# Kernel optimization log

Measured on AMD Instinct MI355X. Metric: run time of the kernel, lower is better.

Reference implementation:

```python
import jax, jax.numpy as jnp
import numpy as np
from jax import lax

B, T, D, H, O = 256, 256, 128, 1024, 128


def setup_inputs() -> dict:
    key = jax.random.key(0)
    ks = jax.random.split(key, 13)
    s = 1.0 / np.sqrt(H)  # torch LSTMCell/Linear init scale
    return {
        "x": jax.random.normal(ks[0], (B, T, D), jnp.float32),
        "h0": jax.random.normal(ks[1], (B, H), jnp.float32),
        "c0": jax.random.normal(ks[2], (B, H), jnp.float32),
        "W_ih0": jax.random.uniform(ks[3], (4 * H, D), jnp.float32, -s, s),
        "W_hh0": jax.random.uniform(ks[4], (4 * H, H), jnp.float32, -s, s),
        "b_ih0": jax.random.uniform(ks[5], (4 * H,), jnp.float32, -s, s),
        "b_hh0": jax.random.uniform(ks[6], (4 * H,), jnp.float32, -s, s),
        "W_ih1": jax.random.uniform(ks[7], (4 * H, H), jnp.float32, -s, s),
        "W_hh1": jax.random.uniform(ks[8], (4 * H, H), jnp.float32, -s, s),
        "b_ih1": jax.random.uniform(ks[9], (4 * H,), jnp.float32, -s, s),
        "b_hh1": jax.random.uniform(ks[10], (4 * H,), jnp.float32, -s, s),
        "W_out": jax.random.uniform(ks[11], (O, H), jnp.float32, -s, s),
        "b_out": jax.random.uniform(ks[12], (O,), jnp.float32, -s, s),
    }


def _lstm_cell(xin, h, c, W_ih, W_hh, b_ih, b_hh):
    # gates in torch order: input, forget, cell(g), output
    g = xin @ W_ih.T + b_ih + h @ W_hh.T + b_hh  # [B, 4H]
    i, f, gg, o = jnp.split(g, 4, axis=-1)
    c_new = jax.nn.sigmoid(f) * c + jax.nn.sigmoid(i) * jnp.tanh(gg)
    h_new = jax.nn.sigmoid(o) * jnp.tanh(c_new)
    return h_new, c_new


def reference(x, h0, c0, W_ih0, W_hh0, b_ih0, b_hh0,
              W_ih1, W_hh1, b_ih1, b_hh1, W_out, b_out):
    xt = jnp.transpose(x, (1, 0, 2))  # [T, B, D] time-major

    def step(carry, xin):
        (ha, ca), (hb, cb) = carry
        ha, ca = _lstm_cell(xin, ha, ca, W_ih0, W_hh0, b_ih0, b_hh0)
        hb, cb = _lstm_cell(ha, hb, cb, W_ih1, W_hh1, b_ih1, b_hh1)
        return ((ha, ca), (hb, cb)), None

    # same initial (h, c) tuple replicated to both layers, as in the original
    init = ((h0, c0), (h0, c0))
    carry, _ = lax.scan(step, init, xt)
    h_last = carry[1][0]  # top-layer hidden at final step, [B, H]
    return h_last @ W_out.T + b_out  # [B, O]
```

## Files before the change

### kernel.cpp

```cpp
#include <hip/hip_runtime.h>
#include <hip/hip_fp16.h>


#define Bq 256
#define Hq 1024

typedef _Float16 half8 __attribute__((ext_vector_type(8)));
typedef float    floatx4 __attribute__((ext_vector_type(4)));

#define N_W1 8388608LL
#define N_W0 4718592LL
#define N_XH 8388608LL
#define N_H  262144LL
#define BH   262144

#define OFF_W1 0LL
#define OFF_W0 16777216LL
#define OFF_XH 26214400LL
#define OFF_BA 42991616LL
#define OFF_BB 44040192LL
#define OFF_HF 45088768LL
#define OFF_SY 46137344LL
#define REQ_WS 46139392LL

__global__ void ws_sentinel_kernel(float* __restrict__ out, int n, float v)
{
    int i = blockIdx.x * blockDim.x + threadIdx.x;
    if (i < n) out[i] = v;
}

__global__ void prep_kernel(const float* __restrict__ x, const float* __restrict__ h0,
                            const float* __restrict__ Wih0, const float* __restrict__ Whh0,
                            const float* __restrict__ Wih1, const float* __restrict__ Whh1,
                            _Float16* __restrict__ w1p, _Float16* __restrict__ w0p,
                            _Float16* __restrict__ xh,
                            _Float16* __restrict__ bufA, _Float16* __restrict__ bufB,
                            unsigned* __restrict__ sync)
{
    long long gid = (long long)blockIdx.x * blockDim.x + threadIdx.x;
    if (gid < 512) sync[gid] = 0u;

    if (gid < N_W1) {
        long long i = gid;
        int e  = (int)(i & 7);
        int jj = (int)((i >> 3) & 15);
        int n  = (int)((i >> 7) & 1);
        int kb = (int)((i >> 8) & 3);
        int ks = (int)((i >> 10) & 63);
        int cb = (int)(i >> 16);
        int row = (2 * n + (jj >> 3)) * 1024 + cb * 8 + (jj & 7);
        int k = ks * 32 + kb * 8 + e;
        float v = (k < 1024) ? Wih1[(size_t)row * 1024 + k]
                             : Whh1[(size_t)row * 1024 + (k - 1024)];
        w1p[i] = (_Float16)v;
    } else if (gid < N_W1 + N_W0) {
        long long i = gid - N_W1;
        int cb = (int)(i / 36864LL);
        int r  = (int)(i - (long long)cb * 36864LL);
        int ks = r >> 10;
        int kb = (r >> 8) & 3;
        int n  = (r >> 7) & 1;
        int jj = (r >> 3) & 15;
        int e  = r & 7;
        int row = (2 * n + (jj >> 3)) * 1024 + cb * 8 + (jj & 7);
        int k = ks * 32 + kb * 8 + e;
        float v = (k < 128) ? Wih0[(size_t)row * 128 + k]
                            : Whh0[(size_t)row * 1024 + (k - 128)];
        w0p[i] = (_Float16)v;
    } else if (gid < N_W1 + N_W0 + N_XH) {
        long long i = gid - N_W1 - N_W0;
        int t    = (int)(i >> 15);
        int rem  = (int)(i & 32767);
        int tile = rem >> 13;
        int b    = (rem >> 5) & 255;
        int e    = rem & 31;
        int d    = tile * 32 + e;
        xh[i] = (_Float16)x[((size_t)b * 256 + t) * 128 + d];
    } else if (gid < N_W1 + N_W0 + N_XH + N_H) {
        long long i = gid - N_W1 - N_W0 - N_XH;
        int row = (int)(i >> 10);
        int j   = (int)(i & 1023);
        size_t idx = (size_t)(j >> 5) * 8192 + (size_t)row * 32 + (j & 31);
        _Float16 v = (_Float16)h0[i];
        bufA[BH + idx] = v;
        bufB[BH + idx] = v;
    }
}

__device__ __forceinline__ void phasebar(unsigned* flags, unsigned* xcdgo,
                                         int bid, int slot, unsigned target)
{
    __builtin_amdgcn_s_waitcnt(0);
    __syncthreads();
    if (threadIdx.x == 0)
        __hip_atomic_store(flags + bid, target, __ATOMIC_RELAXED,
                           __HIP_MEMORY_SCOPE_AGENT);
    if (slot == 0) {
        if (threadIdx.x < 256) {
            int guard = 0;
            while (__hip_atomic_load(flags + threadIdx.x, __ATOMIC_RELAXED,
                                     __HIP_MEMORY_SCOPE_AGENT) < target) {
                __builtin_amdgcn_s_sleep(1);
                if (++guard > (1 << 18)) break;
            }
        }
        __syncthreads();
        if (threadIdx.x < 64) {
            __builtin_amdgcn_fence(__ATOMIC_ACQUIRE, "agent");
            asm volatile("s_waitcnt vmcnt(0) lgkmcnt(0)" ::: "memory");
            if (threadIdx.x == 0)
                __hip_atomic_store(xcdgo, target, __ATOMIC_RELAXED,
                                   __HIP_MEMORY_SCOPE_AGENT);
        }
        __syncthreads();
    } else {
        if (threadIdx.x == 0) {
            int guard = 0;
            while (__hip_atomic_load(xcdgo, __ATOMIC_RELAXED,
                                     __HIP_MEMORY_SCOPE_AGENT) < target) {
                __builtin_amdgcn_s_sleep(1);
                if (++guard > (1 << 18)) break;
            }
        }
        __syncthreads();
        if (threadIdx.x == 0) {
            asm volatile("buffer_inv" ::: "memory");
            asm volatile("s_waitcnt vmcnt(0)" ::: "memory");
        }
        __syncthreads();
    }
}

#define MFMA16(A, Bv, C) __builtin_amdgcn_mfma_f32_16x16x32_f16((A), (Bv), (C), 0, 0, 0)

#define PISSUE(I, P0, P1)                                           \
    asm volatile("global_load_dwordx4 %0, %2, off\n\t"              \
                 "global_load_dwordx4 %1, %3, off"                  \
                 : "=&v"(bf[I][0]), "=&v"(bf[I][1])                 \
                 : "v"(P0), "v"(P1) : "memory")

#define PSTEP22(I, P0, P1) do {                                     \
    half8 b0 = *(const half8*)(bp);                                 \
    half8 b1 = *(const half8*)(bp + 128);                           \
    asm volatile("s_waitcnt vmcnt(22)" ::: "memory");               \
    __builtin_amdgcn_sched_barrier(0);                              \
    acc[0][0] = MFMA16(bf[I][0], b0, acc[0][0]);                    \
    acc[0][1] = MFMA16(bf[I][0], b1, acc[0][1]);                    \
    acc[1][0] = MFMA16(bf[I][1], b0, acc[1][0]);                    \
    acc[1][1] = MFMA16(bf[I][1], b1, acc[1][1]);                    \
    bp += 1024;                                                     \
    PISSUE(I, P0, P1);                                              \
} while (0)

#define PSTEPW(I, NLIT) do {                                        \
    half8 b0 = *(const half8*)(bp);                                 \
    half8 b1 = *(const half8*)(bp + 128);                           \
    asm volatile("s_waitcnt vmcnt(" #NLIT ")" ::: "memory");        \
    __builtin_amdgcn_sched_barrier(0);                              \
    acc[0][0] = MFMA16(bf[I][0], b0, acc[0][0]);                    \
    acc[0][1] = MFMA16(bf[I][0], b1, acc[0][1]);                    \
    acc[1][0] = MFMA16(bf[I][1], b0, acc[1][0]);                    \
    acc[1][1] = MFMA16(bf[I][1], b1, acc[1][1]);                    \
    bp += 1024;                                                     \
} while (0)

__global__ void __launch_bounds__(512)
lstm_main(const _Float16* __restrict__ w1p, const _Float16* __restrict__ w0p,
          const _Float16* __restrict__ xh,
          _Float16* __restrict__ bufA, _Float16* __restrict__ bufB,
          float* __restrict__ hbF,
          const float* __restrict__ c0,
          const float* __restrict__ bih0, const float* __restrict__ bhh0,
          const float* __restrict__ bih1, const float* __restrict__ bhh1,
          const float* __restrict__ Wout, const float* __restrict__ bout,
          float* __restrict__ out, unsigned* __restrict__ sync)
{
    __shared__ _Float16 wlds[65536];

    const int tid  = threadIdx.x;
    const int lane = tid & 63;
    const int w    = tid >> 6;
    const int bid  = blockIdx.x;
    const int xcd  = bid & 7;
    const int slot = bid >> 3;
    const int isL1 = ((slot & 1) == 0);
    const int cb   = xcd * 16 + (slot >> 1);
    const int jbase = cb * 8;
    const int jj = lane & 15;
    const int kb = lane >> 4;
    const int jh = jj & 7;
    const int lo = (jj < 8);
    const int rowbase = w * 32;

    unsigned* xcdgo = sync + 256 + xcd * 16;

    const int jtile = cb >> 2;
    const int jcol  = (cb & 3) * 8 + jh;

    {
        const _Float16* src = isL1 ? (w1p + (size_t)cb * 65536)
                                   : (w0p + (size_t)cb * 36864);
        const int nch = isL1 ? 8192 : 4608;
        for (int i = tid; i < nch; i += 512)
            *(half8*)&wlds[(size_t)i * 8] = *(const half8*)&src[(size_t)i * 8];
    }
    __syncthreads();

    const float* bi  = isL1 ? bih1 : bih0;
    const float* bhp = isL1 ? bhh1 : bhh0;
    float bias[4];
#pragma unroll
    for (int g = 0; g < 4; ++g)
        bias[g] = bi[g * 1024 + jbase + jh] + bhp[g * 1024 + jbase + jh];

    float cc[2][4];
#pragma unroll
    for (int mf = 0; mf < 2; ++mf)
#pragma unroll
        for (int r = 0; r < 4; ++r)
            cc[mf][r] = c0[(size_t)(rowbase + mf * 16 + kb * 4 + r) * Hq + jbase + jh];

    floatx4 acc[2][2];
    half8 bf[12][2];

    for (int t = -1; t <= 255; ++t) {
        const int active = isL1 ? (t >= 0) : (t < 255);
        if (active) {
#pragma unroll
            for (int mf = 0; mf < 2; ++mf)
#pragma unroll
                for (int n = 0; n < 2; ++n)
                    acc[mf][n] = (floatx4){0.f, 0.f, 0.f, 0.f};

            const _Float16* bp = wlds + kb * 256 + jj * 8;
            const size_t loff = (size_t)(rowbase + jj) * 32 + kb * 8;

            if (isL1) {
                const _Float16* apA = bufA + (size_t)(t & 1) * BH + loff;
                const _Float16* apB = bufB + (size_t)((t + 1) & 1) * BH + loff;
#define L1P0(S) (((S) < 32) ? (apA + (size_t)(S) * 8192) : (apB + (size_t)((S) - 32) * 8192))
#define L1P1(S) (L1P0(S) + 512)
#pragma unroll
                for (int i = 0; i < 12; ++i) PISSUE(i, L1P0(i), L1P1(i));
#pragma unroll
                for (int s = 0; s < 52; ++s)
                    PSTEP22(s % 12, L1P0(s + 12), L1P1(s + 12));
                PSTEPW(4, 22);  PSTEPW(5, 20);  PSTEPW(6, 18);  PSTEPW(7, 16);
                PSTEPW(8, 14);  PSTEPW(9, 12);  PSTEPW(10, 10); PSTEPW(11, 8);
                PSTEPW(0, 6);   PSTEPW(1, 4);   PSTEPW(2, 2);   PSTEPW(3, 0);
#undef L1P0
#undef L1P1
            } else {
                const _Float16* apX = xh + (size_t)(t + 1) * 32768 + loff;
                const _Float16* apA = bufA + (size_t)(t & 1) * BH + loff;
#define L0P0(S) (((S) < 4) ? (apX + (size_t)(S) * 8192) : (apA + (size_t)((S) - 4) * 8192))
#define L0P1(S) (L0P0(S) + 512)
#pragma unroll
                for (int i = 0; i < 12; ++i) PISSUE(i, L0P0(i), L0P1(i));
#pragma unroll
                for (int s = 0; s < 24; ++s)
                    PSTEP22(s % 12, L0P0(s + 12), L0P1(s + 12));
                PSTEPW(0, 22);  PSTEPW(1, 20);  PSTEPW(2, 18);  PSTEPW(3, 16);
                PSTEPW(4, 14);  PSTEPW(5, 12);  PSTEPW(6, 10);  PSTEPW(7, 8);
                PSTEPW(8, 6);   PSTEPW(9, 4);   PSTEPW(10, 2);  PSTEPW(11, 0);
#undef L0P0
#undef L0P1
            }

            _Float16* hb = isL1 ? (bufB + (size_t)(t & 1) * BH)
                                : (bufA + (size_t)((t + 1) & 1) * BH);
            unsigned* hb32 = (unsigned*)hb;
#pragma unroll
            for (int mf = 0; mf < 2; ++mf) {
#pragma unroll
                for (int r = 0; r < 4; ++r) {
                    float o0 = acc[mf][0][r];
                    float o1 = acc[mf][1][r];
                    float p0 = __shfl_xor(o0, 8);
                    float p1 = __shfl_xor(o1, 8);
                    float gi = (lo ? o0 : p0) + bias[0];
                    float gf = (lo ? p0 : o0) + bias[1];
                    float gg = (lo ? o1 : p1) + bias[2];
                    float go = (lo ? p1 : o1) + bias[3];
                    float ii = 1.f / (1.f + expf(-gi));
                    float ff = 1.f / (1.f + expf(-gf));
                    float gt = tanhf(gg);
                    float oo = 1.f / (1.f + expf(-go));
                    float cn = ff * cc[mf][r] + ii * gt;
                    cc[mf][r] = cn;
                    float hn = oo * tanhf(cn);

                    union { _Float16 f; unsigned short u; } cv;
                    cv.f = (_Float16)hn;
                    int prt = __shfl_xor((int)cv.u, 1);
                    int row = rowbase + mf * 16 + kb * 4 + r;
                    if (lo && ((jh & 1) == 0)) {
                        unsigned word = (unsigned)cv.u | ((unsigned)prt << 16);
                        size_t eidx = (size_t)jtile * 8192 + (size_t)row * 32 + jcol;
                        __hip_atomic_store(hb32 + (eidx >> 1), word,
                                           __ATOMIC_RELAXED,
                                           __HIP_MEMORY_SCOPE_AGENT);
                    }
                    if (lo && isL1 && t == 255)
                        __hip_atomic_store(hbF + (size_t)row * Hq + jbase + jh,
                                           hn, __ATOMIC_RELAXED,
                                           __HIP_MEMORY_SCOPE_AGENT);
                }
            }
        }

        phasebar(sync, xcdgo, bid, slot, (unsigned)(t + 2));
    }

    int gid = bid * 512 + tid;
    if (gid < Bq * 128) {
        int b = gid >> 7, o = gid & 127;
        const floatx4* hr = (const floatx4*)(hbF + (size_t)b * Hq);
        const floatx4* wr = (const floatx4*)(Wout + (size_t)o * Hq);
        float s = bout[o];
#pragma unroll 4
        for (int k = 0; k < Hq / 4; ++k) {
            floatx4 hv = hr[k], wv = wr[k];
            s += hv[0] * wv[0] + hv[1] * wv[1] + hv[2] * wv[2] + hv[3] * wv[3];
        }
        out[gid] = s;
    }
}

extern "C" void kernel_launch(void* const* d_in, const int* in_sizes, int n_in,
                              void* d_out, int out_size, void* d_ws, size_t ws_size,
                              hipStream_t stream)
{
    (void)in_sizes; (void)n_in;
    float* out = (float*)d_out;

    if (ws_size < (size_t)REQ_WS) {
        float v = -(float)(ws_size >> 20);
        hipLaunchKernelGGL(ws_sentinel_kernel, dim3((out_size + 255) / 256), dim3(256),
                           0, stream, out, out_size, v);
        return;
    }

    const float* x    = (const float*)d_in[0];
    const float* h0   = (const float*)d_in[1];
    const float* c0   = (const float*)d_in[2];
    const float* Wih0 = (const float*)d_in[3];
    const float* Whh0 = (const float*)d_in[4];
    const float* bih0 = (const float*)d_in[5];
    const float* bhh0 = (const float*)d_in[6];
    const float* Wih1 = (const float*)d_in[7];
    const float* Whh1 = (const float*)d_in[8];
    const float* bih1 = (const float*)d_in[9];
    const float* bhh1 = (const float*)d_in[10];
    const float* Wout = (const float*)d_in[11];
    const float* bout = (const float*)d_in[12];

    char* ws = (char*)d_ws;
    _Float16* w1p  = (_Float16*)(ws + OFF_W1);
    _Float16* w0p  = (_Float16*)(ws + OFF_W0);
    _Float16* xh   = (_Float16*)(ws + OFF_XH);
    _Float16* bufA = (_Float16*)(ws + OFF_BA);
    _Float16* bufB = (_Float16*)(ws + OFF_BB);
    float*    hbF  = (float*)   (ws + OFF_HF);
    unsigned* sync = (unsigned*)(ws + OFF_SY);

    long long total = N_W1 + N_W0 + N_XH + N_H;
    hipLaunchKernelGGL(prep_kernel, dim3((unsigned)(total / 256)), dim3(256), 0, stream,
                       x, h0, Wih0, Whh0, Wih1, Whh1, w1p, w0p, xh, bufA, bufB, sync);

    hipLaunchKernelGGL(lstm_main, dim3(256), dim3(512), 0, stream,
                       w1p, w0p, xh, bufA, bufB, hbF, c0,
                       bih0, bhh0, bih1, bhh1, Wout, bout, out, sync);
}
```

Before: 5.233 ms.

## Make grid barrier hierarchical per XCD and use plain stores for hidden state

The grid-wide barrier becomes two-level. Each XCD leader polls only the 32 flags of its own XCD, publishes an XCD-arrived flag, then polls the 8 XCD flags before releasing its local blocks. This replaces one leader per XCD polling all 256 block flags, which was meant to cut cross-die polling traffic. Hidden-state writes switch from relaxed agent-scope atomics to plain stores, relying on the barrier's waitcnt, fence and buffer_inv for visibility. That reliance risks coherence problems if plain stores stay in non-coherent caches.

Result: slower. 5.354 ms (+2.3%).

```diff
diff --git a/kernel.cpp b/kernel.cpp
--- a/kernel.cpp
+++ b/kernel.cpp
@@ -87,18 +87,36 @@
     }
 }
 
-__device__ __forceinline__ void phasebar(unsigned* flags, unsigned* xcdgo,
-                                         int bid, int slot, unsigned target)
+__device__ __forceinline__ void phasebar(unsigned* sync, int xcd, int slot,
+                                         unsigned target)
 {
     __builtin_amdgcn_s_waitcnt(0);
     __syncthreads();
     if (threadIdx.x == 0)
-        __hip_atomic_store(flags + bid, target, __ATOMIC_RELAXED,
+        __hip_atomic_store(sync + xcd * 32 + slot, target, __ATOMIC_RELAXED,
                            __HIP_MEMORY_SCOPE_AGENT);
     if (slot == 0) {
-        if (threadIdx.x < 256) {
+        unsigned* arr = sync + xcd * 32;
+        if (threadIdx.x < 32) {
             int guard = 0;
-            while (__hip_atomic_load(flags + threadIdx.x, __ATOMIC_RELAXED,
+            while (__hip_atomic_load(arr + threadIdx.x, __ATOMIC_RELAXED,
+                                     __HIP_MEMORY_SCOPE_AGENT) < target) {
+                __builtin_amdgcn_s_sleep(1);
+                if (++guard > (1 << 18)) break;
+            }
+        }
+        __syncthreads();
+        if (threadIdx.x < 64) {
+            __builtin_amdgcn_fence(__ATOMIC_RELEASE, "agent");
+            asm volatile("s_waitcnt vmcnt(0) lgkmcnt(0)" ::: "memory");
+            if (threadIdx.x == 0)
+                __hip_atomic_store(sync + 256 + xcd * 16, target,
+                                   __ATOMIC_RELAXED, __HIP_MEMORY_SCOPE_AGENT);
+        }
+        if (threadIdx.x < 8) {
+            int guard = 0;
+            while (__hip_atomic_load(sync + 256 + (int)threadIdx.x * 16,
+                                     __ATOMIC_RELAXED,
                                      __HIP_MEMORY_SCOPE_AGENT) < target) {
                 __builtin_amdgcn_s_sleep(1);
                 if (++guard > (1 << 18)) break;
@@ -109,14 +127,14 @@
             __builtin_amdgcn_fence(__ATOMIC_ACQUIRE, "agent");
             asm volatile("s_waitcnt vmcnt(0) lgkmcnt(0)" ::: "memory");
             if (threadIdx.x == 0)
-                __hip_atomic_store(xcdgo, target, __ATOMIC_RELAXED,
-                                   __HIP_MEMORY_SCOPE_AGENT);
+                __hip_atomic_store(sync + 384 + xcd * 16, target,
+                                   __ATOMIC_RELAXED, __HIP_MEMORY_SCOPE_AGENT);
         }
         __syncthreads();
     } else {
         if (threadIdx.x == 0) {
             int guard = 0;
-            while (__hip_atomic_load(xcdgo, __ATOMIC_RELAXED,
+            while (__hip_atomic_load(sync + 384 + xcd * 16, __ATOMIC_RELAXED,
                                      __HIP_MEMORY_SCOPE_AGENT) < target) {
                 __builtin_amdgcn_s_sleep(1);
                 if (++guard > (1 << 18)) break;
@@ -191,8 +209,6 @@
     const int jh = jj & 7;
     const int lo = (jj < 8);
     const int rowbase = w * 32;
-
-    unsigned* xcdgo = sync + 256 + xcd * 16;
 
     const int jtile = cb >> 2;
     const int jcol  = (cb & 3) * 8 + jh;
@@ -297,19 +313,15 @@
                     if (lo && ((jh & 1) == 0)) {
                         unsigned word = (unsigned)cv.u | ((unsigned)prt << 16);
                         size_t eidx = (size_t)jtile * 8192 + (size_t)row * 32 + jcol;
-                        __hip_atomic_store(hb32 + (eidx >> 1), word,
-                                           __ATOMIC_RELAXED,
-                                           __HIP_MEMORY_SCOPE_AGENT);
+                        hb32[eidx >> 1] = word;
                     }
                     if (lo && isL1 && t == 255)
-                        __hip_atomic_store(hbF + (size_t)row * Hq + jbase + jh,
-                                           hn, __ATOMIC_RELAXED,
-                                           __HIP_MEMORY_SCOPE_AGENT);
+                        hbF[(size_t)row * Hq + jbase + jh] = hn;
                 }
             }
         }
 
-        phasebar(sync, xcdgo, bid, slot, (unsigned)(t + 2));
+        phasebar(sync, xcd, slot, (unsigned)(t + 2));
     }
 
     int gid = bid * 512 + tid;
```
